# Performance work log

Hardware: AMD Instinct MI355X
Metric: run time of the kernel (lower is better)

The kernel has to match this reference:

```python
import jax, jax.numpy as jnp
import numpy as np

N_NODES = 100000
N_EDGES = 3200000
IN_C = 256
HID = 32
OUT_C = 64


def setup_inputs() -> dict:
    key = jax.random.key(0)
    ks = jax.random.split(key, 12)
    x = jax.random.normal(ks[0], (N_NODES, IN_C), dtype=jnp.float32)
    edge_index = jax.random.randint(ks[1], (2, N_EDGES), 0, N_NODES, dtype=jnp.int64)

    def lin(kw, kb, fan_in, fan_out):
        bound = 1.0 / np.sqrt(fan_in)
        W = jax.random.uniform(kw, (fan_out, fan_in), jnp.float32, -bound, bound)
        b = jax.random.uniform(kb, (fan_out,), jnp.float32, -bound, bound)
        return W, b

    W0, b0 = lin(ks[2], ks[3], IN_C, HID)
    W1, b1 = lin(ks[4], ks[5], HID, HID)
    W2, b2 = lin(ks[6], ks[7], HID, HID)
    W3, b3 = lin(ks[8], ks[9], HID, HID)
    W4, b4 = lin(ks[10], ks[11], HID, OUT_C)
    return {"x": x, "edge_index": edge_index,
            "W0": W0, "b0": b0, "W1": W1, "b1": b1, "W2": W2, "b2": b2,
            "W3": W3, "b3": b3, "W4": W4, "b4": b4}


def _gcn_norm(edge_index, num_nodes):
    # add self loops, symmetric normalization (PyG gcn_norm, edge_weight = 1)
    loop = jnp.arange(num_nodes, dtype=edge_index.dtype)
    row = jnp.concatenate([edge_index[0], loop])  # source nodes
    col = jnp.concatenate([edge_index[1], loop])  # target nodes
    deg = jax.ops.segment_sum(jnp.ones_like(col, dtype=jnp.float32), col,
                              num_segments=num_nodes)
    dinv = jnp.where(deg > 0, jax.lax.rsqrt(jnp.maximum(deg, 1e-12)), 0.0)
    norm = dinv[row] * dinv[col]
    return row, col, norm


def reference(x, edge_index, W0, b0, W1, b1, W2, b2, W3, b3, W4, b4):
    row, col, norm = _gcn_norm(edge_index, N_NODES)

    def prop(h):
        # gather source features, scale by norm, scatter-add to targets
        return jax.ops.segment_sum(norm[:, None] * h[row], col,
                                   num_segments=N_NODES)

    def sgconv(h, W, b):  # SGConv with K=1: propagate then linear
        return prop(h) @ W.T + b

    h = x @ W0.T + b0
    h = jax.nn.relu(sgconv(h, W1, b1))
    h = jax.nn.relu(sgconv(h, W2, b2))
    h = jax.nn.relu(sgconv(h, W3, b3))
    return h @ W4.T + b4
```

## Files before the change

kernel.cpp:

```cpp
#include <hip/hip_runtime.h>
#include <hip/hip_fp16.h>

#define N_NODES 100000
#define N_EDGES 3200000
#define IN_C 256
#define HID 32
#define OUT_C 64
#define CAP 80
#define NP 100032
#define BINW 256
#define BSH 8
#define NBIN 391
#define BCHUNK 8192

typedef _Float16 f16x8 __attribute__((ext_vector_type(8)));
typedef float f32x4 __attribute__((ext_vector_type(4)));

__device__ __forceinline__ float dot4(const float4 a, const float4 b) {
    return a.x * b.x + a.y * b.y + a.z * b.z + a.w * b.w;
}

__device__ __forceinline__ float4 h4tof4(uint2 v) {
    __half2 a = *reinterpret_cast<__half2*>(&v.x);
    __half2 b = *reinterpret_cast<__half2*>(&v.y);
    float2 fa = __half22float2(a), fb = __half22float2(b);
    return make_float4(fa.x, fa.y, fb.x, fb.y);
}
__device__ __forceinline__ uint2 f4toh4(float4 f) {
    __half2 a = __float22half2_rn(make_float2(f.x, f.y));
    __half2 b = __float22half2_rn(make_float2(f.z, f.w));
    uint2 v;
    v.x = *reinterpret_cast<unsigned int*>(&a);
    v.y = *reinterpret_cast<unsigned int*>(&b);
    return v;
}


__global__ __launch_bounds__(256) void k_binhist(const int* __restrict__ col,
                                                 int* __restrict__ binCnt) {
    __shared__ int h[NBIN];
    const int t = threadIdx.x;
    for (int i = t; i < NBIN; i += 256) h[i] = 0;
    __syncthreads();
    const long e0 = (long)blockIdx.x * BCHUNK;
    const long e1 = min((long)N_EDGES, e0 + BCHUNK);
    for (long i = e0 + t; i < e1; i += 256)
        atomicAdd(&h[col[i] >> BSH], 1);
    __syncthreads();
    for (int i = t; i < NBIN; i += 256)
        if (h[i]) atomicAdd(&binCnt[i], h[i]);
}

__global__ void k_binscan(const int* __restrict__ binCnt,
                          int* __restrict__ binStart, int* __restrict__ binCursor) {
    __shared__ int buf[2][512];
    const int t = threadIdx.x;
    int v = (t < NBIN) ? binCnt[t] : 0;
    buf[0][t] = v;
    __syncthreads();
    int s = 0;
    for (int off = 1; off < 512; off <<= 1) {
        int d = s ^ 1;
        int val = buf[s][t];
        if (t >= off) val += buf[s][t - off];
        buf[d][t] = val;
        __syncthreads();
        s = d;
    }
    if (t < NBIN) {
        int st = buf[s][t] - v;
        binStart[t] = st;
        binCursor[t] = st;
    }
}

__global__ __launch_bounds__(256) void k_binscatter(const int* __restrict__ row,
                                                    const int* __restrict__ col,
                                                    int* __restrict__ binCursor,
                                                    int2* __restrict__ pairs) {
    __shared__ int cnt[NBIN];
    __shared__ int ofs[NBIN];
    const int t = threadIdx.x;
    for (int i = t; i < NBIN; i += 256) cnt[i] = 0;
    __syncthreads();
    const long e0 = (long)blockIdx.x * BCHUNK;
    const long e1 = min((long)N_EDGES, e0 + BCHUNK);
    for (long i = e0 + t; i < e1; i += 256)
        atomicAdd(&cnt[col[i] >> BSH], 1);
    __syncthreads();
    for (int i = t; i < NBIN; i += 256) {
        int c = cnt[i];
        ofs[i] = c ? atomicAdd(&binCursor[i], c) : 0;
        cnt[i] = 0;
    }
    __syncthreads();
    for (long i = e0 + t; i < e1; i += 256) {
        int c = col[i];
        int b = c >> BSH;
        int p = ofs[b] + atomicAdd(&cnt[b], 1);
        pairs[p] = make_int2(row[i], c);
    }
}

__global__ __launch_bounds__(256) void k_binbuild(const int2* __restrict__ pairs,
                                                  const int* __restrict__ binStart,
                                                  const int* __restrict__ binCnt,
                                                  int* __restrict__ bucket,
                                                  int* __restrict__ degc,
                                                  float* __restrict__ dinv) {
    __shared__ int cur[BINW];
    const int t = threadIdx.x;
    const int bin = blockIdx.x;
    const int base = bin * BINW;
    cur[t] = 0;
    __syncthreads();
    const int s = binStart[bin], cn = binCnt[bin];
    for (int i = t; i < cn; i += 256) {
        int2 e = pairs[s + i];
        int c = e.y - base;
        int pos = atomicAdd(&cur[c], 1);
        if (pos < CAP) bucket[(size_t)(base + c) * CAP + pos] = e.x;
    }
    __syncthreads();
    int n = base + t;
    if (n < N_NODES) {
        int d = cur[t];
        degc[n] = d;
        dinv[n] = 1.0f / sqrtf((float)(d + 1));
    }
}


__global__ void k_hist(const int* __restrict__ col, int* __restrict__ deg) {
    int i = blockIdx.x * 256 + threadIdx.x;
    if (i < N_EDGES) atomicAdd(&deg[col[i]], 1);
}

__global__ void k_scan1(const int* __restrict__ deg, int* __restrict__ rowptr,
                        int* __restrict__ bsum) {
    __shared__ int buf[2][1024];
    const int t = threadIdx.x, b = blockIdx.x;
    const int i = b * 1024 + t;
    int v = (i < N_NODES) ? deg[i] : 0;
    buf[0][t] = v;
    __syncthreads();
    int src = 0;
    for (int off = 1; off < 1024; off <<= 1) {
        int dst = src ^ 1;
        int val = buf[src][t];
        if (t >= off) val += buf[src][t - off];
        buf[dst][t] = val;
        __syncthreads();
        src = dst;
    }
    int incl = buf[src][t];
    if (i < N_NODES) rowptr[i] = incl - v;
    if (t == 1023) bsum[b] = incl;
}

__global__ void k_scan2(int* __restrict__ bsum, int nb) {
    __shared__ int buf[2][128];
    const int t = threadIdx.x;
    int v = (t < nb) ? bsum[t] : 0;
    buf[0][t] = v;
    __syncthreads();
    int src = 0;
    for (int off = 1; off < 128; off <<= 1) {
        int dst = src ^ 1;
        int val = buf[src][t];
        if (t >= off) val += buf[src][t - off];
        buf[dst][t] = val;
        __syncthreads();
        src = dst;
    }
    if (t < nb) bsum[t] = buf[src][t] - v;
}

__global__ void k_scan3(int* __restrict__ rowptr, const int* __restrict__ bsum) {
    int i = blockIdx.x * 256 + threadIdx.x;
    if (i < N_NODES) rowptr[i] += bsum[i >> 10];
}

__global__ void k_dinv(const int* __restrict__ cnt, int stride,
                       float* __restrict__ dinv, int* __restrict__ degc) {
    int i = blockIdx.x * 256 + threadIdx.x;
    if (i < N_NODES) {
        int d = cnt[i * stride];
        degc[i] = d;
        dinv[i] = 1.0f / sqrtf((float)(d + 1));
    }
}

__global__ void k_scatter(const int* __restrict__ row, const int* __restrict__ col,
                          const int* __restrict__ rowptr, int* __restrict__ cursor,
                          int* __restrict__ csr) {
    int i = blockIdx.x * 256 + threadIdx.x;
    if (i < N_EDGES) {
        int c = col[i];
        int pos = rowptr[c] + atomicAdd(&cursor[c], 1);
        csr[pos] = row[i];
    }
}

__global__ __launch_bounds__(256) void k_lin0_mfma(
        const float* __restrict__ x,
        const float* __restrict__ W0,
        const float* __restrict__ b0,
        const float* __restrict__ dinv,
        uint2* __restrict__ g2) {
    __shared__ f16x8 WH[1024];
    __shared__ f16x8 WL[1024];

    const int t = threadIdx.x;
    const int w = t >> 6;
    const int l = t & 63;
    const int lr = l & 15;
    const int lg = l >> 4;

    for (int s = t; s < 1024; s += 256) {
        const int lane = s & 63;
        const int mtks = s >> 6;
        const int ks = mtks & 7, mt = mtks >> 3;
        const float* wr = W0 + (size_t)(mt * 16 + (lane & 15)) * IN_C
                             + ks * 32 + (lane >> 4) * 8;
        float4 a0 = *(const float4*)(wr);
        float4 a1 = *(const float4*)(wr + 4);
        float v[8] = {a0.x, a0.y, a0.z, a0.w, a1.x, a1.y, a1.z, a1.w};
        f16x8 h, lo;
        #pragma unroll
        for (int e = 0; e < 8; ++e) {
            float sv = v[e] * 16.0f;
            _Float16 hh = (_Float16)sv;
            h[e] = hh;
            lo[e] = (_Float16)(sv - (float)hh);
        }
        WH[s] = h;
        WL[s] = lo;
    }
    __syncthreads();

    const int unit = blockIdx.x * 4 + w;
    if (unit * 32 >= N_NODES) return;
    const int n0 = unit * 32;

    f32x4 acc[2][2];
    #pragma unroll
    for (int mt = 0; mt < 2; ++mt)
        #pragma unroll
        for (int nt = 0; nt < 2; ++nt)
            acc[mt][nt] = (f32x4){0.f, 0.f, 0.f, 0.f};

    const float* xr0 = x + (size_t)(n0 + lr) * IN_C + lg * 8;
    const float* xr1 = x + (size_t)(n0 + 16 + lr) * IN_C + lg * 8;

    #pragma unroll
    for (int ks = 0; ks < 8; ++ks) {
        float4 u0 = *(const float4*)(xr0 + ks * 32);
        float4 u1 = *(const float4*)(xr0 + ks * 32 + 4);
        float4 v0 = *(const float4*)(xr1 + ks * 32);
        float4 v1 = *(const float4*)(xr1 + ks * 32 + 4);
        float fu[8] = {u0.x, u0.y, u0.z, u0.w, u1.x, u1.y, u1.z, u1.w};
        float fv[8] = {v0.x, v0.y, v0.z, v0.w, v1.x, v1.y, v1.z, v1.w};
        f16x8 xh0, xl0, xh1, xl1;
        #pragma unroll
        for (int e = 0; e < 8; ++e) {
            _Float16 h0 = (_Float16)fu[e];
            xh0[e] = h0;
            xl0[e] = (_Float16)(fu[e] - (float)h0);
            _Float16 h1 = (_Float16)fv[e];
            xh1[e] = h1;
            xl1[e] = (_Float16)(fv[e] - (float)h1);
        }
        #pragma unroll
        for (int mt = 0; mt < 2; ++mt) {
            f16x8 wh = WH[mt * 512 + ks * 64 + l];
            f16x8 wl = WL[mt * 512 + ks * 64 + l];
            acc[mt][0] = __builtin_amdgcn_mfma_f32_16x16x32_f16(wh, xh0, acc[mt][0], 0, 0, 0);
            acc[mt][0] = __builtin_amdgcn_mfma_f32_16x16x32_f16(wh, xl0, acc[mt][0], 0, 0, 0);
            acc[mt][0] = __builtin_amdgcn_mfma_f32_16x16x32_f16(wl, xh0, acc[mt][0], 0, 0, 0);
            acc[mt][1] = __builtin_amdgcn_mfma_f32_16x16x32_f16(wh, xh1, acc[mt][1], 0, 0, 0);
            acc[mt][1] = __builtin_amdgcn_mfma_f32_16x16x32_f16(wh, xl1, acc[mt][1], 0, 0, 0);
            acc[mt][1] = __builtin_amdgcn_mfma_f32_16x16x32_f16(wl, xh1, acc[mt][1], 0, 0, 0);
        }
    }

    #pragma unroll
    for (int nt = 0; nt < 2; ++nt) {
        const int node = n0 + nt * 16 + lr;
        const float dv = dinv[node];
        #pragma unroll
        for (int mt = 0; mt < 2; ++mt) {
            const float4 bb = *(const float4*)(b0 + mt * 16 + lg * 4);
            f32x4 a = acc[mt][nt];
            float4 r = make_float4((a[0] * 0.0625f + bb.x) * dv,
                                   (a[1] * 0.0625f + bb.y) * dv,
                                   (a[2] * 0.0625f + bb.z) * dv,
                                   (a[3] * 0.0625f + bb.w) * dv);
            g2[(size_t)node * 8 + mt * 4 + lg] = f4toh4(r);
        }
    }
}


__global__ __launch_bounds__(256) void k_prop2(
        const uint2* __restrict__ g2, const int* __restrict__ idx,
        const int* __restrict__ base_arr,
        const int* __restrict__ cnt_arr, int maxcnt,
        const float* __restrict__ dinv,
        const float* __restrict__ W, const float* __restrict__ b,
        uint2* __restrict__ gout2) {
    __shared__ float4 Ws[HID * 9];
    const int t = threadIdx.x;
    { int c = t >> 3, k4 = t & 7; Ws[c * 9 + k4] = ((const float4*)W)[t]; }
    __syncthreads();

    const int l = t & 7;
    const int n = blockIdx.x * 32 + (t >> 3);
    if (n >= N_NODES) return;

    int cnt = cnt_arr[n];
    if (cnt > maxcnt) cnt = maxcnt;
    const int base = base_arr ? base_arr[n] : n * CAP;
    const int* __restrict__ e = idx + base;

    float4 acc = h4tof4(g2[n * 8 + l]);
    int j = 0;
    for (; j + 8 <= cnt; j += 8) {
        int r0 = e[j], r1 = e[j + 1], r2 = e[j + 2], r3 = e[j + 3];
        int r4 = e[j + 4], r5 = e[j + 5], r6 = e[j + 6], r7 = e[j + 7];
        uint2 v0 = g2[r0 * 8 + l], v1 = g2[r1 * 8 + l];
        uint2 v2 = g2[r2 * 8 + l], v3 = g2[r3 * 8 + l];
        uint2 v4 = g2[r4 * 8 + l], v5 = g2[r5 * 8 + l];
        uint2 v6 = g2[r6 * 8 + l], v7 = g2[r7 * 8 + l];
        float4 a0 = h4tof4(v0), a1 = h4tof4(v1), a2 = h4tof4(v2), a3 = h4tof4(v3);
        float4 a4 = h4tof4(v4), a5 = h4tof4(v5), a6 = h4tof4(v6), a7 = h4tof4(v7);
        acc.x += a0.x + a1.x + a2.x + a3.x + a4.x + a5.x + a6.x + a7.x;
        acc.y += a0.y + a1.y + a2.y + a3.y + a4.y + a5.y + a6.y + a7.y;
        acc.z += a0.z + a1.z + a2.z + a3.z + a4.z + a5.z + a6.z + a7.z;
        acc.w += a0.w + a1.w + a2.w + a3.w + a4.w + a5.w + a6.w + a7.w;
    }
    for (; j < cnt; ++j) {
        float4 a = h4tof4(g2[e[j] * 8 + l]);
        acc.x += a.x; acc.y += a.y; acc.z += a.z; acc.w += a.w;
    }

    const float dv = dinv[n];
    float4 y = make_float4(0.f, 0.f, 0.f, 0.f);
    #pragma unroll
    for (int m = 0; m < 8; ++m) {
        float4 sv;
        sv.x = __shfl(acc.x, m, 8);
        sv.y = __shfl(acc.y, m, 8);
        sv.z = __shfl(acc.z, m, 8);
        sv.w = __shfl(acc.w, m, 8);
        y.x += dot4(Ws[(4 * l + 0) * 9 + m], sv);
        y.y += dot4(Ws[(4 * l + 1) * 9 + m], sv);
        y.z += dot4(Ws[(4 * l + 2) * 9 + m], sv);
        y.w += dot4(Ws[(4 * l + 3) * 9 + m], sv);
    }
    const float4 bb = ((const float4*)b)[l];
    y.x = fmaxf(bb.x + dv * y.x, 0.f) * dv;
    y.y = fmaxf(bb.y + dv * y.y, 0.f) * dv;
    y.z = fmaxf(bb.z + dv * y.z, 0.f) * dv;
    y.w = fmaxf(bb.w + dv * y.w, 0.f) * dv;
    gout2[n * 8 + l] = f4toh4(y);
}

__global__ __launch_bounds__(256) void k_last2(
        const uint2* __restrict__ g2, const int* __restrict__ idx,
        const int* __restrict__ base_arr,
        const int* __restrict__ cnt_arr, int maxcnt,
        const float* __restrict__ dinv,
        const float* __restrict__ W3, const float* __restrict__ b3,
        const float* __restrict__ W4, const float* __restrict__ b4,
        float4* __restrict__ out4) {
    __shared__ float4 W3s[HID * 9];
    __shared__ float4 W4s[OUT_C * 9];
    const int t = threadIdx.x;
    { int c = t >> 3, k4 = t & 7; W3s[c * 9 + k4] = ((const float4*)W3)[t]; }
    #pragma unroll
    for (int f = t; f < 512; f += 256) {
        int c = f >> 3, k4 = f & 7;
        W4s[c * 9 + k4] = ((const float4*)W4)[f];
    }
    __syncthreads();

    const int l = t & 7;
    const int n = blockIdx.x * 32 + (t >> 3);
    if (n >= N_NODES) return;

    int cnt = cnt_arr[n];
    if (cnt > maxcnt) cnt = maxcnt;
    const int base = base_arr ? base_arr[n] : n * CAP;
    const int* __restrict__ e = idx + base;

    float4 acc = h4tof4(g2[n * 8 + l]);
    int j = 0;
    for (; j + 8 <= cnt; j += 8) {
        int r0 = e[j], r1 = e[j + 1], r2 = e[j + 2], r3 = e[j + 3];
        int r4 = e[j + 4], r5 = e[j + 5], r6 = e[j + 6], r7 = e[j + 7];
        uint2 v0 = g2[r0 * 8 + l], v1 = g2[r1 * 8 + l];
        uint2 v2 = g2[r2 * 8 + l], v3 = g2[r3 * 8 + l];
        uint2 v4 = g2[r4 * 8 + l], v5 = g2[r5 * 8 + l];
        uint2 v6 = g2[r6 * 8 + l], v7 = g2[r7 * 8 + l];
        float4 a0 = h4tof4(v0), a1 = h4tof4(v1), a2 = h4tof4(v2), a3 = h4tof4(v3);
        float4 a4 = h4tof4(v4), a5 = h4tof4(v5), a6 = h4tof4(v6), a7 = h4tof4(v7);
        acc.x += a0.x + a1.x + a2.x + a3.x + a4.x + a5.x + a6.x + a7.x;
        acc.y += a0.y + a1.y + a2.y + a3.y + a4.y + a5.y + a6.y + a7.y;
        acc.z += a0.z + a1.z + a2.z + a3.z + a4.z + a5.z + a6.z + a7.z;
        acc.w += a0.w + a1.w + a2.w + a3.w + a4.w + a5.w + a6.w + a7.w;
    }
    for (; j < cnt; ++j) {
        float4 a = h4tof4(g2[e[j] * 8 + l]);
        acc.x += a.x; acc.y += a.y; acc.z += a.z; acc.w += a.w;
    }

    const float dv = dinv[n];
    float4 y = make_float4(0.f, 0.f, 0.f, 0.f);
    #pragma unroll
    for (int m = 0; m < 8; ++m) {
        float4 sv;
        sv.x = __shfl(acc.x, m, 8);
        sv.y = __shfl(acc.y, m, 8);
        sv.z = __shfl(acc.z, m, 8);
        sv.w = __shfl(acc.w, m, 8);
        y.x += dot4(W3s[(4 * l + 0) * 9 + m], sv);
        y.y += dot4(W3s[(4 * l + 1) * 9 + m], sv);
        y.z += dot4(W3s[(4 * l + 2) * 9 + m], sv);
        y.w += dot4(W3s[(4 * l + 3) * 9 + m], sv);
    }
    const float4 b3v = ((const float4*)b3)[l];
    float4 h;
    h.x = fmaxf(b3v.x + dv * y.x, 0.f);
    h.y = fmaxf(b3v.y + dv * y.y, 0.f);
    h.z = fmaxf(b3v.z + dv * y.z, 0.f);
    h.w = fmaxf(b3v.w + dv * y.w, 0.f);

    float4 ya = make_float4(0.f, 0.f, 0.f, 0.f);
    float4 yb = make_float4(0.f, 0.f, 0.f, 0.f);
    #pragma unroll
    for (int m = 0; m < 8; ++m) {
        float4 hv;
        hv.x = __shfl(h.x, m, 8);
        hv.y = __shfl(h.y, m, 8);
        hv.z = __shfl(h.z, m, 8);
        hv.w = __shfl(h.w, m, 8);
        ya.x += dot4(W4s[(4 * l + 0) * 9 + m], hv);
        ya.y += dot4(W4s[(4 * l + 1) * 9 + m], hv);
        ya.z += dot4(W4s[(4 * l + 2) * 9 + m], hv);
        ya.w += dot4(W4s[(4 * l + 3) * 9 + m], hv);
        yb.x += dot4(W4s[(32 + 4 * l + 0) * 9 + m], hv);
        yb.y += dot4(W4s[(32 + 4 * l + 1) * 9 + m], hv);
        yb.z += dot4(W4s[(32 + 4 * l + 2) * 9 + m], hv);
        yb.w += dot4(W4s[(32 + 4 * l + 3) * 9 + m], hv);
    }
    const float4 b4a = ((const float4*)b4)[l];
    const float4 b4b = ((const float4*)b4)[8 + l];
    ya.x += b4a.x; ya.y += b4a.y; ya.z += b4a.z; ya.w += b4a.w;
    yb.x += b4b.x; yb.y += b4b.y; yb.z += b4b.z; yb.w += b4b.w;
    out4[n * 16 + l] = ya;
    out4[n * 16 + 8 + l] = yb;
}


extern "C" void kernel_launch(void* const* d_in, const int* in_sizes, int n_in,
                              void* d_out, int out_size, void* d_ws, size_t ws_size,
                              hipStream_t stream) {
    const float* x   = (const float*)d_in[0];
    const int*   ei  = (const int*)d_in[1];
    const int*   row = ei;
    const int*   col = ei + N_EDGES;
    const float* W0 = (const float*)d_in[2];
    const float* b0 = (const float*)d_in[3];
    const float* W1 = (const float*)d_in[4];
    const float* b1 = (const float*)d_in[5];
    const float* W2 = (const float*)d_in[6];
    const float* b2 = (const float*)d_in[7];
    const float* W3 = (const float*)d_in[8];
    const float* b3 = (const float*)d_in[9];
    const float* W4 = (const float*)d_in[10];
    const float* b4 = (const float*)d_in[11];
    float* out = (float*)d_out;

    const int EB = (N_EDGES + 255) / 256;
    const int NB256 = (N_NODES + 255) / 256;
    const int NB1024 = (N_NODES + 1023) / 1024;
    const int CB = (N_EDGES + BCHUNK - 1) / BCHUNK;
    const int UNITS = (N_NODES + 31) / 32;
    const int LB0 = (UNITS + 3) / 4;
    const int PB2 = (N_NODES + 31) / 32;

    const size_t UNION_BYTES = (size_t)N_EDGES * sizeof(int2);
    const size_t FAST_BYTES =
        (size_t)N_NODES * CAP * 4 + 2ull * NP * 4 + 3ull * 512 * 4 + UNION_BYTES;

    if (ws_size >= FAST_BYTES) {
        int*   bucket    = (int*)d_ws;
        float* dinv      = (float*)(bucket + (size_t)N_NODES * CAP);
        int*   degc      = (int*)(dinv + NP);
        int*   binCnt    = degc + NP;
        int*   binStart  = binCnt + 512;
        int*   binCursor = binStart + 512;
        char*  uni       = (char*)(binCursor + 512);
        int2*  pairs     = (int2*)uni;
        uint2* gA        = (uint2*)uni;
        uint2* gB        = gA + (size_t)N_NODES * 8;

        hipMemsetAsync(binCnt, 0, 512 * sizeof(int), stream);
        k_binhist<<<CB, 256, 0, stream>>>(col, binCnt);
        k_binscan<<<1, 512, 0, stream>>>(binCnt, binStart, binCursor);
        k_binscatter<<<CB, 256, 0, stream>>>(row, col, binCursor, pairs);
        k_binbuild<<<NBIN, 256, 0, stream>>>(pairs, binStart, binCnt,
                                             bucket, degc, dinv);

        k_lin0_mfma<<<LB0, 256, 0, stream>>>(x, W0, b0, dinv, gA);

        k_prop2<<<PB2, 256, 0, stream>>>(gA, bucket, nullptr, degc, CAP,
                                         dinv, W1, b1, gB);
        k_prop2<<<PB2, 256, 0, stream>>>(gB, bucket, nullptr, degc, CAP,
                                         dinv, W2, b2, gA);
        k_last2<<<PB2, 256, 0, stream>>>(gA, bucket, nullptr, degc, CAP,
                                         dinv, W3, b3, W4, b4, (float4*)out);
    } else {
        int*   deg    = (int*)d_ws;
        int*   rowptr = deg + NP;
        int*   cursor = rowptr + NP;
        int*   bsum   = cursor + NP;
        float* dinv   = (float*)(bsum + 128);
        int*   csr    = (int*)(dinv + NP);
        uint2* gA     = (uint2*)(csr + N_EDGES);
        uint2* gB     = gA + (size_t)N_NODES * 8;

        hipMemsetAsync(deg, 0, (size_t)NP * 3 * sizeof(int), stream);
        k_hist<<<EB, 256, 0, stream>>>(col, deg);
        k_scan1<<<NB1024, 1024, 0, stream>>>(deg, rowptr, bsum);
        k_scan2<<<1, 128, 0, stream>>>(bsum, NB1024);
        k_scan3<<<NB256, 256, 0, stream>>>(rowptr, bsum);
        k_dinv<<<NB256, 256, 0, stream>>>(deg, 1, dinv, cursor);
        hipMemsetAsync(cursor, 0, (size_t)NP * sizeof(int), stream);
        k_scatter<<<EB, 256, 0, stream>>>(row, col, rowptr, cursor, csr);

        k_lin0_mfma<<<LB0, 256, 0, stream>>>(x, W0, b0, dinv, gA);

        k_prop2<<<PB2, 256, 0, stream>>>(gA, csr, rowptr, deg, 1 << 30,
                                         dinv, W1, b1, gB);
        k_prop2<<<PB2, 256, 0, stream>>>(gB, csr, rowptr, deg, 1 << 30,
                                         dinv, W2, b2, gA);
        k_last2<<<PB2, 256, 0, stream>>>(gA, csr, rowptr, deg, 1 << 30,
                                         dinv, W3, b3, W4, b4, (float4*)out);
    }
}
```

Measured before the change: 465.9 us.

## Use split-fp16 MFMA for propagation layers' dense transforms

Replaces the fast-path propagation kernels with versions where each wavefront handles 16 nodes. Each lane gathers 8 fp16 features per neighbor with 16-byte loads and accumulates in fp32. The per-node 32x32 (and final 32x64) linear layers then run on MFMA 16x16x32 fp16 instructions instead of scalar FMA with LDS-staged weights. Accuracy is kept by splitting weights and activations into high and low fp16 parts (three MFMAs per tile), and the fused final layer is reshuffled through lane shuffles. The aim is to cut scalar ALU work and widen the gather loads, at the cost of more complex data movement and a slight change in rounding.

Result: faster. 452.9 us (-2.8%).

```diff
diff --git a/kernel.cpp b/kernel.cpp
--- a/kernel.cpp
+++ b/kernel.cpp
@@ -33,6 +33,22 @@
     v.x = *reinterpret_cast<unsigned int*>(&a);
     v.y = *reinterpret_cast<unsigned int*>(&b);
     return v;
+}
+
+__device__ __forceinline__ void h8acc(uint4 v, float* acc) {
+    __half2* p = reinterpret_cast<__half2*>(&v);
+    #pragma unroll
+    for (int i = 0; i < 4; ++i) {
+        float2 f = __half22float2(p[i]);
+        acc[2 * i] += f.x;
+        acc[2 * i + 1] += f.y;
+    }
+}
+
+__device__ __forceinline__ unsigned packh2(_Float16 a, _Float16 b) {
+    unsigned short ua = __builtin_bit_cast(unsigned short, a);
+    unsigned short ub = __builtin_bit_cast(unsigned short, b);
+    return (unsigned)ua | ((unsigned)ub << 16);
 }
 
 
@@ -301,6 +317,262 @@
     }
 }
 
+__global__ __launch_bounds__(256) void k_prop_mfma(
+        const uint2* __restrict__ g2, const int* __restrict__ idx,
+        const int* __restrict__ cnt_arr,
+        const float* __restrict__ dinv,
+        const float* __restrict__ W, const float* __restrict__ b,
+        uint2* __restrict__ gout2) {
+    __shared__ f16x8 WH[128], WL[128];
+    const int t = threadIdx.x;
+    if (t < 128) {
+        const int lane = t & 63, mt = t >> 6;
+        const float* wr = W + (size_t)(mt * 16 + (lane & 15)) * HID + (lane >> 4) * 8;
+        f16x8 h, lo;
+        #pragma unroll
+        for (int e = 0; e < 8; ++e) {
+            float sv = wr[e] * 8.0f;
+            _Float16 hh = (_Float16)sv;
+            h[e] = hh;
+            lo[e] = (_Float16)(sv - (float)hh);
+        }
+        WH[t] = h;
+        WL[t] = lo;
+    }
+    __syncthreads();
+
+    const int l = t & 63;
+    const int tile = blockIdx.x * 4 + (t >> 6);
+    const int n0 = tile * 16;
+    if (n0 >= N_NODES) return;
+    const int node = n0 + (l & 15);
+    const int lg = l >> 4;
+
+    const uint4* __restrict__ g4 = (const uint4*)g2;
+    float acc[8];
+    #pragma unroll
+    for (int i = 0; i < 8; ++i) acc[i] = 0.f;
+    h8acc(g4[(size_t)node * 4 + lg], acc);
+
+    const int cn = min(cnt_arr[node], CAP);
+    const int* __restrict__ e = idx + (size_t)node * CAP;
+    int j = 0;
+    for (; j + 8 <= cn; j += 8) {
+        int4 ra = *(const int4*)(e + j);
+        int4 rb = *(const int4*)(e + j + 4);
+        uint4 v0 = g4[(size_t)ra.x * 4 + lg];
+        uint4 v1 = g4[(size_t)ra.y * 4 + lg];
+        uint4 v2 = g4[(size_t)ra.z * 4 + lg];
+        uint4 v3 = g4[(size_t)ra.w * 4 + lg];
+        uint4 v4 = g4[(size_t)rb.x * 4 + lg];
+        uint4 v5 = g4[(size_t)rb.y * 4 + lg];
+        uint4 v6 = g4[(size_t)rb.z * 4 + lg];
+        uint4 v7 = g4[(size_t)rb.w * 4 + lg];
+        h8acc(v0, acc); h8acc(v1, acc); h8acc(v2, acc); h8acc(v3, acc);
+        h8acc(v4, acc); h8acc(v5, acc); h8acc(v6, acc); h8acc(v7, acc);
+    }
+    for (; j < cn; ++j) h8acc(g4[(size_t)e[j] * 4 + lg], acc);
+
+    f16x8 bh, bl;
+    #pragma unroll
+    for (int i = 0; i < 8; ++i) {
+        _Float16 hh = (_Float16)acc[i];
+        bh[i] = hh;
+        bl[i] = (_Float16)(acc[i] - (float)hh);
+    }
+
+    f32x4 c0 = (f32x4){0.f, 0.f, 0.f, 0.f};
+    f32x4 c1 = (f32x4){0.f, 0.f, 0.f, 0.f};
+    {
+        f16x8 wh0 = WH[l], wl0 = WL[l];
+        f16x8 wh1 = WH[64 + l], wl1 = WL[64 + l];
+        c0 = __builtin_amdgcn_mfma_f32_16x16x32_f16(wh0, bh, c0, 0, 0, 0);
+        c0 = __builtin_amdgcn_mfma_f32_16x16x32_f16(wh0, bl, c0, 0, 0, 0);
+        c0 = __builtin_amdgcn_mfma_f32_16x16x32_f16(wl0, bh, c0, 0, 0, 0);
+        c1 = __builtin_amdgcn_mfma_f32_16x16x32_f16(wh1, bh, c1, 0, 0, 0);
+        c1 = __builtin_amdgcn_mfma_f32_16x16x32_f16(wh1, bl, c1, 0, 0, 0);
+        c1 = __builtin_amdgcn_mfma_f32_16x16x32_f16(wl1, bh, c1, 0, 0, 0);
+    }
+
+    const float dv = dinv[node];
+    #pragma unroll
+    for (int mt = 0; mt < 2; ++mt) {
+        const f32x4 bb = *(const f32x4*)(b + mt * 16 + lg * 4);
+        f32x4 a = mt ? c1 : c0;
+        float4 r;
+        r.x = fmaxf(bb[0] + dv * (a[0] * 0.125f), 0.f) * dv;
+        r.y = fmaxf(bb[1] + dv * (a[1] * 0.125f), 0.f) * dv;
+        r.z = fmaxf(bb[2] + dv * (a[2] * 0.125f), 0.f) * dv;
+        r.w = fmaxf(bb[3] + dv * (a[3] * 0.125f), 0.f) * dv;
+        gout2[(size_t)node * 8 + mt * 4 + lg] = f4toh4(r);
+    }
+}
+
+__global__ __launch_bounds__(256) void k_last_mfma(
+        const uint2* __restrict__ g2, const int* __restrict__ idx,
+        const int* __restrict__ cnt_arr,
+        const float* __restrict__ dinv,
+        const float* __restrict__ W3, const float* __restrict__ b3,
+        const float* __restrict__ W4, const float* __restrict__ b4,
+        float4* __restrict__ out4) {
+    __shared__ f16x8 WH3[128], WL3[128];
+    __shared__ f16x8 WH4[256], WL4[256];
+    const int t = threadIdx.x;
+    if (t < 128) {
+        const int lane = t & 63, mt = t >> 6;
+        const float* wr = W3 + (size_t)(mt * 16 + (lane & 15)) * HID + (lane >> 4) * 8;
+        f16x8 h, lo;
+        #pragma unroll
+        for (int e = 0; e < 8; ++e) {
+            float sv = wr[e] * 8.0f;
+            _Float16 hh = (_Float16)sv;
+            h[e] = hh;
+            lo[e] = (_Float16)(sv - (float)hh);
+        }
+        WH3[t] = h;
+        WL3[t] = lo;
+    }
+    {
+        const int lane = t & 63, mt = t >> 6;
+        const float* wr = W4 + (size_t)(mt * 16 + (lane & 15)) * HID + (lane >> 4) * 8;
+        f16x8 h, lo;
+        #pragma unroll
+        for (int e = 0; e < 8; ++e) {
+            float sv = wr[e] * 8.0f;
+            _Float16 hh = (_Float16)sv;
+            h[e] = hh;
+            lo[e] = (_Float16)(sv - (float)hh);
+        }
+        WH4[t] = h;
+        WL4[t] = lo;
+    }
+    __syncthreads();
+
+    const int l = t & 63;
+    const int tile = blockIdx.x * 4 + (t >> 6);
+    const int n0 = tile * 16;
+    if (n0 >= N_NODES) return;
+    const int nl = l & 15;
+    const int node = n0 + nl;
+    const int lg = l >> 4;
+
+    const uint4* __restrict__ g4 = (const uint4*)g2;
+    float acc[8];
+    #pragma unroll
+    for (int i = 0; i < 8; ++i) acc[i] = 0.f;
+    h8acc(g4[(size_t)node * 4 + lg], acc);
+
+    const int cn = min(cnt_arr[node], CAP);
+    const int* __restrict__ e = idx + (size_t)node * CAP;
+    int j = 0;
+    for (; j + 8 <= cn; j += 8) {
+        int4 ra = *(const int4*)(e + j);
+        int4 rb = *(const int4*)(e + j + 4);
+        uint4 v0 = g4[(size_t)ra.x * 4 + lg];
+        uint4 v1 = g4[(size_t)ra.y * 4 + lg];
+        uint4 v2 = g4[(size_t)ra.z * 4 + lg];
+        uint4 v3 = g4[(size_t)ra.w * 4 + lg];
+        uint4 v4 = g4[(size_t)rb.x * 4 + lg];
+        uint4 v5 = g4[(size_t)rb.y * 4 + lg];
+        uint4 v6 = g4[(size_t)rb.z * 4 + lg];
+        uint4 v7 = g4[(size_t)rb.w * 4 + lg];
+        h8acc(v0, acc); h8acc(v1, acc); h8acc(v2, acc); h8acc(v3, acc);
+        h8acc(v4, acc); h8acc(v5, acc); h8acc(v6, acc); h8acc(v7, acc);
+    }
+    for (; j < cn; ++j) h8acc(g4[(size_t)e[j] * 4 + lg], acc);
+
+    f16x8 bh, bl;
+    #pragma unroll
+    for (int i = 0; i < 8; ++i) {
+        _Float16 hh = (_Float16)acc[i];
+        bh[i] = hh;
+        bl[i] = (_Float16)(acc[i] - (float)hh);
+    }
+
+    f32x4 c0 = (f32x4){0.f, 0.f, 0.f, 0.f};
+    f32x4 c1 = (f32x4){0.f, 0.f, 0.f, 0.f};
+    {
+        f16x8 wh0 = WH3[l], wl0 = WL3[l];
+        f16x8 wh1 = WH3[64 + l], wl1 = WL3[64 + l];
+        c0 = __builtin_amdgcn_mfma_f32_16x16x32_f16(wh0, bh, c0, 0, 0, 0);
+        c0 = __builtin_amdgcn_mfma_f32_16x16x32_f16(wh0, bl, c0, 0, 0, 0);
+        c0 = __builtin_amdgcn_mfma_f32_16x16x32_f16(wl0, bh, c0, 0, 0, 0);
+        c1 = __builtin_amdgcn_mfma_f32_16x16x32_f16(wh1, bh, c1, 0, 0, 0);
+        c1 = __builtin_amdgcn_mfma_f32_16x16x32_f16(wh1, bl, c1, 0, 0, 0);
+        c1 = __builtin_amdgcn_mfma_f32_16x16x32_f16(wl1, bh, c1, 0, 0, 0);
+    }
+
+    const float dv = dinv[node];
+    const f32x4 b3a = *(const f32x4*)(b3 + lg * 4);
+    const f32x4 b3b = *(const f32x4*)(b3 + 16 + lg * 4);
+    float h0[4], h1[4];
+    #pragma unroll
+    for (int r = 0; r < 4; ++r) {
+        h0[r] = fmaxf(b3a[r] + dv * (c0[r] * 0.125f), 0.f);
+        h1[r] = fmaxf(b3b[r] + dv * (c1[r] * 0.125f), 0.f);
+    }
+
+    unsigned ph[2][2], pl_[2][2];
+    #pragma unroll
+    for (int p = 0; p < 2; ++p) {
+        _Float16 a0 = (_Float16)h0[2 * p], a1 = (_Float16)h0[2 * p + 1];
+        _Float16 l0 = (_Float16)(h0[2 * p] - (float)a0);
+        _Float16 l1 = (_Float16)(h0[2 * p + 1] - (float)a1);
+        ph[0][p] = packh2(a0, a1);
+        pl_[0][p] = packh2(l0, l1);
+        _Float16 c0_ = (_Float16)h1[2 * p], c1_ = (_Float16)h1[2 * p + 1];
+        _Float16 d0 = (_Float16)(h1[2 * p] - (float)c0_);
+        _Float16 d1 = (_Float16)(h1[2 * p + 1] - (float)c1_);
+        ph[1][p] = packh2(c0_, c1_);
+        pl_[1][p] = packh2(d0, d1);
+    }
+
+    union { unsigned u[4]; f16x8 v; } Bh, Bl;
+    #pragma unroll
+    for (int q = 0; q < 4; ++q) {
+        int src = nl + 16 * ((lg & 1) * 2 + (q >> 1));
+        unsigned a0 = (unsigned)__shfl((int)ph[0][q & 1], src, 64);
+        unsigned a1 = (unsigned)__shfl((int)ph[1][q & 1], src, 64);
+        Bh.u[q] = (lg >= 2) ? a1 : a0;
+        unsigned c0_ = (unsigned)__shfl((int)pl_[0][q & 1], src, 64);
+        unsigned c1_ = (unsigned)__shfl((int)pl_[1][q & 1], src, 64);
+        Bl.u[q] = (lg >= 2) ? c1_ : c0_;
+    }
+
+    f32x4 o0 = (f32x4){0.f, 0.f, 0.f, 0.f};
+    f32x4 o1 = (f32x4){0.f, 0.f, 0.f, 0.f};
+    f32x4 o2 = (f32x4){0.f, 0.f, 0.f, 0.f};
+    f32x4 o3 = (f32x4){0.f, 0.f, 0.f, 0.f};
+    {
+        f16x8 wh, wl;
+        wh = WH4[l];        wl = WL4[l];
+        o0 = __builtin_amdgcn_mfma_f32_16x16x32_f16(wh, Bh.v, o0, 0, 0, 0);
+        o0 = __builtin_amdgcn_mfma_f32_16x16x32_f16(wh, Bl.v, o0, 0, 0, 0);
+        o0 = __builtin_amdgcn_mfma_f32_16x16x32_f16(wl, Bh.v, o0, 0, 0, 0);
+        wh = WH4[64 + l];   wl = WL4[64 + l];
+        o1 = __builtin_amdgcn_mfma_f32_16x16x32_f16(wh, Bh.v, o1, 0, 0, 0);
+        o1 = __builtin_amdgcn_mfma_f32_16x16x32_f16(wh, Bl.v, o1, 0, 0, 0);
+        o1 = __builtin_amdgcn_mfma_f32_16x16x32_f16(wl, Bh.v, o1, 0, 0, 0);
+        wh = WH4[128 + l];  wl = WL4[128 + l];
+        o2 = __builtin_amdgcn_mfma_f32_16x16x32_f16(wh, Bh.v, o2, 0, 0, 0);
+        o2 = __builtin_amdgcn_mfma_f32_16x16x32_f16(wh, Bl.v, o2, 0, 0, 0);
+        o2 = __builtin_amdgcn_mfma_f32_16x16x32_f16(wl, Bh.v, o2, 0, 0, 0);
+        wh = WH4[192 + l];  wl = WL4[192 + l];
+        o3 = __builtin_amdgcn_mfma_f32_16x16x32_f16(wh, Bh.v, o3, 0, 0, 0);
+        o3 = __builtin_amdgcn_mfma_f32_16x16x32_f16(wh, Bl.v, o3, 0, 0, 0);
+        o3 = __builtin_amdgcn_mfma_f32_16x16x32_f16(wl, Bh.v, o3, 0, 0, 0);
+    }
+
+    #pragma unroll
+    for (int mt = 0; mt < 4; ++mt) {
+        const f32x4 bb = *(const f32x4*)(b4 + mt * 16 + lg * 4);
+        f32x4 a = (mt == 0) ? o0 : (mt == 1) ? o1 : (mt == 2) ? o2 : o3;
+        out4[(size_t)node * 16 + mt * 4 + lg] =
+            make_float4(a[0] * 0.125f + bb[0], a[1] * 0.125f + bb[1],
+                        a[2] * 0.125f + bb[2], a[3] * 0.125f + bb[3]);
+    }
+}
+
 
 __global__ __launch_bounds__(256) void k_prop2(
         const uint2* __restrict__ g2, const int* __restrict__ idx,
@@ -488,6 +760,7 @@
     const int CB = (N_EDGES + BCHUNK - 1) / BCHUNK;
     const int UNITS = (N_NODES + 31) / 32;
     const int LB0 = (UNITS + 3) / 4;
+    const int MB = (N_NODES + 63) / 64;
     const int PB2 = (N_NODES + 31) / 32;
 
     const size_t UNION_BYTES = (size_t)N_EDGES * sizeof(int2);
@@ -515,12 +788,10 @@
 
         k_lin0_mfma<<<LB0, 256, 0, stream>>>(x, W0, b0, dinv, gA);
 
-        k_prop2<<<PB2, 256, 0, stream>>>(gA, bucket, nullptr, degc, CAP,
-                                         dinv, W1, b1, gB);
-        k_prop2<<<PB2, 256, 0, stream>>>(gB, bucket, nullptr, degc, CAP,
-                                         dinv, W2, b2, gA);
-        k_last2<<<PB2, 256, 0, stream>>>(gA, bucket, nullptr, degc, CAP,
-                                         dinv, W3, b3, W4, b4, (float4*)out);
+        k_prop_mfma<<<MB, 256, 0, stream>>>(gA, bucket, degc, dinv, W1, b1, gB);
+        k_prop_mfma<<<MB, 256, 0, stream>>>(gB, bucket, degc, dinv, W2, b2, gA);
+        k_last_mfma<<<MB, 256, 0, stream>>>(gA, bucket, degc, dinv,
+                                            W3, b3, W4, b4, (float4*)out);
     } else {
         int*   deg    = (int*)d_ws;
         int*   rowptr = deg + NP;
```
